# Kernel optimization log

Hardware: AMD Instinct MI355X
Metric: run time of the kernel (lower is better)

The kernel has to match this reference:

```python
import jax, jax.numpy as jnp
import numpy as np

N, C, S, K, H, ES, L = 50000, 128, 2048, 64, 128, 256, 5
E = S * ES


def setup_inputs() -> dict:
    key = jax.random.key(0)
    ks = jax.random.split(key, 16)
    lin = lambda k_, i, o: jax.random.normal(k_, (i, o), jnp.float32) * 0.02
    inp = {}
    inp["x"] = jax.random.normal(ks[0], (N, C), jnp.float32)
    inp["log_probs"] = jax.random.normal(ks[1], (S,), jnp.float32)
    inp["node_proj_w"] = lin(ks[2], C, H); inp["node_proj_b"] = jnp.zeros(H, jnp.float32)
    inp["logp_proj_w"] = lin(ks[3], 1, H); inp["logp_proj_b"] = jnp.zeros(H, jnp.float32)
    inp["root_emb"] = jax.random.normal(ks[4], (2, H), jnp.float32) * 0.02
    inp["init_proj_w"] = lin(ks[5], 3 * H, H); inp["init_proj_b"] = jnp.zeros(H, jnp.float32)
    inp["gin_eps"] = jnp.zeros(L, jnp.float32)
    inp["mlp_w1"] = jax.random.normal(ks[6], (L, H, H), jnp.float32) * 0.02
    inp["mlp_b1"] = jnp.zeros((L, H), jnp.float32)
    inp["mlp_w2"] = jax.random.normal(ks[7], (L, H, H), jnp.float32) * 0.02
    inp["mlp_b2"] = jnp.zeros((L, H), jnp.float32)
    inp["mp2_w"] = jax.random.normal(ks[8], (L, 2 * H, H), jnp.float32) * 0.02
    inp["mp2_b"] = jnp.zeros((L, H), jnp.float32)
    inp["bn_gamma"] = jnp.ones((L, H), jnp.float32)
    inp["bn_beta"] = jnp.zeros((L, H), jnp.float32)
    inp["nodes_t"] = jax.random.randint(ks[9], (S, K), 0, N, jnp.int32)
    inp["root_local"] = jax.random.randint(ks[10], (S,), 0, K, jnp.int32)
    inp["edge_index_t"] = jax.random.randint(ks[11], (2, E), 0, K, jnp.int32)
    inp["edge_ptr"] = jnp.arange(S + 1, dtype=jnp.int32) * ES  # uniform ES edges/subgraph
    return inp


def reference(x, log_probs, node_proj_w, node_proj_b, logp_proj_w, logp_proj_b,
              root_emb, init_proj_w, init_proj_b, gin_eps, mlp_w1, mlp_b1,
              mlp_w2, mlp_b2, mp2_w, mp2_b, bn_gamma, bn_beta,
              nodes_t, root_local, edge_index_t, edge_ptr):
    S_, K_ = nodes_t.shape
    N_total = x.shape[0]
    ids = nodes_t.reshape(-1)                      # [S*k] global IDs, -1 = pad
    valid = ids >= 0
    vf = valid.astype(x.dtype)[:, None]            # [S*k,1]
    idc = jnp.maximum(ids, 0)

    # ---- initial features: node_proj(x_v) || logp_proj(log_p) || root_emb ----
    gx = x[idc] * vf                               # [S*k,C]
    lp = jnp.repeat(log_probs, K_)[:, None]        # [S*k,1]
    root_flat = jnp.arange(S_, dtype=jnp.int32) * K_ + root_local
    root_mask = jnp.zeros(S_ * K_, jnp.int32).at[root_flat].set(1)
    h_node = gx @ node_proj_w + node_proj_b
    h_logp = lp @ logp_proj_w + logp_proj_b
    h_root = root_emb[root_mask]
    h = jnp.concatenate([h_node, h_logp, h_root], axis=-1) @ init_proj_w + init_proj_b

    # ---- intra-subgraph edge index in the flat S*k node space ----
    eidx = jnp.arange(edge_index_t.shape[1], dtype=jnp.int32)
    sub_of_edge = jnp.searchsorted(edge_ptr, eidx, side='right').astype(jnp.int32) - 1
    offs = sub_of_edge * K_
    src = edge_index_t[0] + offs
    dst = edge_index_t[1] + offs

    # valid-node counts per original-graph node (for scatter-mean)
    cnt = jax.ops.segment_sum(vf[:, 0], idc, num_segments=N_total)
    inv_cnt = (1.0 / jnp.maximum(cnt, 1.0))[:, None]

    for l in range(L):
        h_res = h
        # MP-1: GINConv  out = MLP((1+eps)*h + sum_{j->i} h_j)
        agg = jax.ops.segment_sum(h[src], dst, num_segments=S_ * K_)
        z = (1.0 + gin_eps[l]) * h + agg
        z = jax.nn.relu(z @ mlp_w1[l] + mlp_b1[l]) @ mlp_w2[l] + mlp_b2[l]
        # MP-2: cross-subgraph scatter-mean over global node IDs, gather back
        x_agg = jax.ops.segment_sum(z * vf, idc, num_segments=N_total) * inv_cnt
        x_cross = x_agg[idc] * vf
        u = jax.nn.relu(jnp.concatenate([z, x_cross], axis=-1) @ mp2_w[l] + mp2_b[l])
        # BatchNorm (batch statistics, biased var)
        mu = u.mean(axis=0)
        var = u.var(axis=0)
        u = (u - mu) * jax.lax.rsqrt(var + 1e-5) * bn_gamma[l] + bn_beta[l]
        h = u + h_res  # residual; dropout is identity in deterministic reference
    return h
```

## Files before the change

kernel.cpp:

```cpp
#include <hip/hip_runtime.h>
#include <cstdint>

#define NN   50000
#define SS   2048
#define KSUB 64
#define HH   128
#define EE   (SS * 256)
#define SKK  (SS * KSUB)
#define LLAY 5
#define NBLK 196

typedef __attribute__((ext_vector_type(8))) short bhalf8;
typedef __attribute__((ext_vector_type(4))) float f32x4;

__device__ __forceinline__ ushort f2b(float f) {
  uint u = __builtin_bit_cast(uint, f);
  uint r = (u + 0x7FFFu + ((u >> 16) & 1u)) >> 16;
  return (ushort)r;
}
__device__ __forceinline__ float b2f(ushort u) {
  uint v = ((uint)u) << 16;
  return __builtin_bit_cast(float, v);
}
__device__ __forceinline__ void fsplit(float f, ushort& hi, ushort& lo) {
  hi = f2b(f);
  lo = f2b(f - b2f(hi));
}
__device__ __forceinline__ int zoff(int row, int col) {
  return row * 256 + (((col * 2) & 255) ^ ((row & 7) << 4));
}

__global__ void fold_M_k(const float* __restrict__ Wn, const float* __restrict__ Wi,
                         ushort* __restrict__ Mth, ushort* __restrict__ Mtl) {
  int c = blockIdx.x, n = threadIdx.x;
  float s = 0.f;
  for (int k = 0; k < HH; ++k) s = fmaf(Wn[c * HH + k], Wi[k * HH + n], s);
  ushort hi, lo; fsplit(s, hi, lo);
  Mth[n * HH + c] = hi; Mtl[n * HH + c] = lo;
}

__global__ void fold_vec_k(const float* __restrict__ Wi, const float* __restrict__ wl,
                           const float* __restrict__ bnb, const float* __restrict__ blb,
                           const float* __restrict__ bi, const float* __restrict__ remb,
                           float* __restrict__ vl, float* __restrict__ c0,
                           float* __restrict__ rev) {
  int n = threadIdx.x;
  float svl = 0.f, sc0 = bi[n], r0 = 0.f, r1 = 0.f;
  for (int k = 0; k < HH; ++k) {
    svl = fmaf(wl[k], Wi[(HH + k) * HH + n], svl);
    sc0 = fmaf(bnb[k], Wi[k * HH + n], sc0);
    sc0 = fmaf(blb[k], Wi[(HH + k) * HH + n], sc0);
    r0  = fmaf(remb[k],      Wi[(2 * HH + k) * HH + n], r0);
    r1  = fmaf(remb[HH + k], Wi[(2 * HH + k) * HH + n], r1);
  }
  vl[n] = svl; c0[n] = sc0; rev[n] = r0; rev[HH + n] = r1;
}

__global__ void wconv_k(const float* __restrict__ w1, const float* __restrict__ w2,
                        const float* __restrict__ mp2w,
                        ushort* __restrict__ w1th, ushort* __restrict__ w1tl,
                        ushort* __restrict__ w2th, ushort* __restrict__ w2tl,
                        ushort* __restrict__ mp2th, ushort* __restrict__ mp2tl) {
  int b = blockIdx.x, n = threadIdx.x;
  ushort hi, lo;
  if (b < 640) {
    int l = b >> 7, k = b & 127;
    fsplit(w1[((size_t)l * HH + k) * HH + n], hi, lo);
    w1th[((size_t)l * HH + n) * HH + k] = hi;
    w1tl[((size_t)l * HH + n) * HH + k] = lo;
  } else if (b < 1280) {
    int bb = b - 640; int l = bb >> 7, k = bb & 127;
    fsplit(w2[((size_t)l * HH + k) * HH + n], hi, lo);
    w2th[((size_t)l * HH + n) * HH + k] = hi;
    w2tl[((size_t)l * HH + n) * HH + k] = lo;
  } else {
    int bb = b - 1280; int l = bb >> 8, k = bb & 255;
    fsplit(mp2w[((size_t)l * 256 + k) * HH + n], hi, lo);
    mp2th[((size_t)l * HH + n) * 256 + k] = hi;
    mp2tl[((size_t)l * HH + n) * 256 + k] = lo;
  }
}

__global__ void count_k(const int* __restrict__ idc, int* __restrict__ cnt) {
  int i = blockIdx.x * 256 + threadIdx.x;
  if (i < SKK) atomicAdd(&cnt[idc[i]], 1);
}

__global__ void scan1_k(const int* __restrict__ cnt, int* __restrict__ excl,
                        int* __restrict__ bsum) {
  __shared__ int sh[256];
  const int tid = threadIdx.x;
  const int i = blockIdx.x * 256 + tid;
  int v = (i < NN) ? cnt[i] : 0;
  sh[tid] = v;
  __syncthreads();
#pragma unroll
  for (int off = 1; off < 256; off <<= 1) {
    int t = (tid >= off) ? sh[tid - off] : 0;
    __syncthreads();
    sh[tid] += t;
    __syncthreads();
  }
  excl[i] = sh[tid] - v;
  if (tid == 255) bsum[blockIdx.x] = sh[tid];
}

__global__ void scan2_k(int* __restrict__ bsum, int* __restrict__ boff) {
  __shared__ int sh[256];
  const int tid = threadIdx.x;
  int v = (tid < NBLK) ? bsum[tid] : 0;
  sh[tid] = v;
  __syncthreads();
#pragma unroll
  for (int off = 1; off < 256; off <<= 1) {
    int t = (tid >= off) ? sh[tid - off] : 0;
    __syncthreads();
    sh[tid] += t;
    __syncthreads();
  }
  boff[tid] = sh[tid] - v;
}

__global__ void scan3_k(const int* __restrict__ excl, const int* __restrict__ boff,
                        int* __restrict__ node_ptr) {
  int i = blockIdx.x * 256 + threadIdx.x;
  if (i < NN) node_ptr[i] = excl[i] + boff[blockIdx.x];
  if (i == 0) node_ptr[NN] = SKK;
}

__global__ void fill_rows_k(const int* __restrict__ idc, const int* __restrict__ node_ptr,
                            int* __restrict__ cur, int* __restrict__ rowlist) {
  int i = blockIdx.x * 256 + threadIdx.x;
  if (i < SKK) {
    int id = idc[i];
    int pos = atomicAdd(&cur[id], 1);
    rowlist[node_ptr[id] + pos] = i;
  }
}

__launch_bounds__(256)
__global__ void scatter_mean_k(const ushort* __restrict__ zh, const ushort* __restrict__ zl,
                               const int* __restrict__ node_ptr,
                               const int* __restrict__ rowlist,
                               ushort* __restrict__ xah, ushort* __restrict__ xal) {
  const int tid = threadIdx.x;
  const int n = blockIdx.x * 8 + (tid >> 5);
  if (n >= NN) return;
  const int c4 = (tid & 31) * 4;
  const int p0 = node_ptr[n], p1 = node_ptr[n + 1];
  float s0 = 0.f, s1 = 0.f, s2 = 0.f, s3 = 0.f;
  for (int p = p0; p < p1; ++p) {
    const size_t off = (size_t)rowlist[p] * HH + c4;
    uint2 vh = *(const uint2*)(zh + off);
    uint2 vl = *(const uint2*)(zl + off);
    s0 += b2f((ushort)vh.x) + b2f((ushort)vl.x);
    s1 += b2f((ushort)(vh.x >> 16)) + b2f((ushort)(vl.x >> 16));
    s2 += b2f((ushort)vh.y) + b2f((ushort)vl.y);
    s3 += b2f((ushort)(vh.y >> 16)) + b2f((ushort)(vl.y >> 16));
  }
  const float inv = 1.0f / (float)max(p1 - p0, 1);
  ushort h0, l0, h1, l1, h2, l2, h3, l3;
  fsplit(s0 * inv, h0, l0); fsplit(s1 * inv, h1, l1);
  fsplit(s2 * inv, h2, l2); fsplit(s3 * inv, h3, l3);
  uint2 oh, ol;
  oh.x = (uint)h0 | ((uint)h1 << 16); oh.y = (uint)h2 | ((uint)h3 << 16);
  ol.x = (uint)l0 | ((uint)l1 << 16); ol.y = (uint)l2 | ((uint)l3 << 16);
  *(uint2*)(xah + (size_t)n * HH + c4) = oh;
  *(uint2*)(xal + (size_t)n * HH + c4) = ol;
}

__launch_bounds__(256)
__global__ void presort_k(const int* __restrict__ e_src, const int* __restrict__ e_dst,
                          const int* __restrict__ edge_ptr, int* __restrict__ row_ptr,
                          int* __restrict__ ssrc) {
  __shared__ int cnt[KSUB];
  __shared__ int base[KSUB];
  __shared__ int cur[KSUB];
  const int s = blockIdx.x, tid = threadIdx.x;
  const int p0 = edge_ptr[s], p1 = edge_ptr[s + 1];
  if (tid < KSUB) cnt[tid] = 0;
  __syncthreads();
  for (int e = p0 + tid; e < p1; e += 256) atomicAdd(&cnt[e_dst[e]], 1);
  __syncthreads();
  if (tid == 0) {
    int a = 0;
    for (int d = 0; d < KSUB; ++d) { base[d] = a; a += cnt[d]; }
  }
  __syncthreads();
  if (tid < KSUB) { row_ptr[s * KSUB + tid] = p0 + base[tid]; cur[tid] = base[tid]; }
  if (s == 0 && tid == 0) row_ptr[SS * KSUB] = edge_ptr[SS];
  __syncthreads();
  for (int e = p0 + tid; e < p1; e += 256) {
    int d = e_dst[e];
    int pos = atomicAdd(&cur[d], 1);
    ssrc[p0 + pos] = e_src[e];
  }
}

template <bool FIRST>
__launch_bounds__(256, 4)
__global__ void gin_mega_k(float* __restrict__ h, const float* __restrict__ uf,
                           const float* __restrict__ stats,
                           const float* __restrict__ gamma, const float* __restrict__ beta,
                           const int* __restrict__ row_ptr, const int* __restrict__ ssrc,
                           const float* __restrict__ gin_eps, const int layer,
                           const ushort* __restrict__ B1h, const ushort* __restrict__ B1l,
                           const ushort* __restrict__ B2h, const ushort* __restrict__ B2l,
                           const float* __restrict__ bias1, const float* __restrict__ bias2,
                           ushort* __restrict__ zh, ushort* __restrict__ zl) {
  constexpr int LDH = 132;
  __shared__ __align__(16) char smem[KSUB * LDH * 4];
  float*  hl = (float*)smem;
  ushort* Zh = (ushort*)smem;
  ushort* Zl = (ushort*)(smem + KSUB * HH * 2);
  const int s = blockIdx.x, tid = threadIdx.x;
  const size_t base = (size_t)s * KSUB * HH;

  float csc[4], csh[4];
  const int cb = (tid * 4) & 127;
  if constexpr (!FIRST) {
    const float invM = 1.0f / (float)SKK;
#pragma unroll
    for (int e = 0; e < 4; ++e) {
      const float mu = stats[cb + e] * invM;
      const float var = fmaf(-mu, mu, stats[HH + cb + e] * invM);
      const float sc = rsqrtf(var + 1e-5f) * gamma[cb + e];
      csc[e] = sc; csh[e] = fmaf(-mu, sc, beta[cb + e]);
    }
  }
#pragma unroll
  for (int it = 0; it < 8; ++it) {
    const int idx = it * 1024 + tid * 4;
    const int m = idx >> 7, c = idx & 127;
    float4 hv = *(const float4*)&h[base + idx];
    if constexpr (!FIRST) {
      float4 u4 = *(const float4*)&uf[base + idx];
      hv.x += fmaf(u4.x, csc[0], csh[0]);
      hv.y += fmaf(u4.y, csc[1], csh[1]);
      hv.z += fmaf(u4.z, csc[2], csh[2]);
      hv.w += fmaf(u4.w, csc[3], csh[3]);
      *(float4*)&h[base + idx] = hv;
    }
    *(float4*)&hl[m * LDH + c] = hv;
  }
  __syncthreads();

  const float ep1 = 1.0f + gin_eps[layer];
  const int d = tid >> 2, q4 = (tid & 3) * 4;
  const int g = s * KSUB + d;
  const int e0 = row_ptr[g], e1 = row_ptr[g + 1];
  float a[32];
  {
    const float* hp0 = &hl[d * LDH + q4];
#pragma unroll
    for (int j = 0; j < 8; ++j) {
      float4 v = *(const float4*)(hp0 + 16 * j);
      a[4 * j + 0] = ep1 * v.x; a[4 * j + 1] = ep1 * v.y;
      a[4 * j + 2] = ep1 * v.z; a[4 * j + 3] = ep1 * v.w;
    }
    for (int e = e0; e < e1; ++e) {
      const float* hp = &hl[ssrc[e] * LDH + q4];
#pragma unroll
      for (int j = 0; j < 8; ++j) {
        float4 v = *(const float4*)(hp + 16 * j);
        a[4 * j + 0] += v.x; a[4 * j + 1] += v.y;
        a[4 * j + 2] += v.z; a[4 * j + 3] += v.w;
      }
    }
  }
  __syncthreads();

#pragma unroll
  for (int j = 0; j < 8; ++j) {
    ushort th[4], tl[4];
#pragma unroll
    for (int k = 0; k < 4; ++k) fsplit(a[4 * j + k], th[k], tl[k]);
    const int o = zoff(d, q4 + 16 * j);
    *(uint2*)((char*)Zh + o) = *(uint2*)th;
    *(uint2*)((char*)Zl + o) = *(uint2*)tl;
  }
  __syncthreads();

  const int lane = tid & 63, wv = tid >> 6;
  const int fr = lane & 15, quad = lane >> 4;
  const int nj0 = wv * 32 + fr, nj1 = nj0 + 16;

  f32x4 acc[4][2];
#pragma unroll
  for (int i = 0; i < 4; ++i) { acc[i][0] = (f32x4){0,0,0,0}; acc[i][1] = (f32x4){0,0,0,0}; }

#pragma unroll
  for (int ch = 0; ch < 4; ++ch) {
    bhalf8 afh[4], afl[4], bfh[2], bfl[2];
#pragma unroll
    for (int i = 0; i < 4; ++i) {
      const int o = zoff(i * 16 + fr, ch * 32 + quad * 8);
      afh[i] = *(const bhalf8*)((const char*)Zh + o);
      afl[i] = *(const bhalf8*)((const char*)Zl + o);
    }
#pragma unroll
    for (int j = 0; j < 2; ++j) {
      const size_t off = (size_t)(wv * 32 + j * 16 + fr) * HH + ch * 32 + quad * 8;
      bfh[j] = *(const bhalf8*)(B1h + off);
      bfl[j] = *(const bhalf8*)(B1l + off);
    }
#pragma unroll
    for (int i = 0; i < 4; ++i)
#pragma unroll
      for (int j = 0; j < 2; ++j) {
        acc[i][j] = __builtin_amdgcn_mfma_f32_16x16x32_bf16(afh[i], bfh[j], acc[i][j], 0, 0, 0);
        acc[i][j] = __builtin_amdgcn_mfma_f32_16x16x32_bf16(afl[i], bfh[j], acc[i][j], 0, 0, 0);
        acc[i][j] = __builtin_amdgcn_mfma_f32_16x16x32_bf16(afh[i], bfl[j], acc[i][j], 0, 0, 0);
      }
  }
  __syncthreads();

  {
    const float b10 = bias1[nj0], b11 = bias1[nj1];
#pragma unroll
    for (int i = 0; i < 4; ++i)
#pragma unroll
      for (int r = 0; r < 4; ++r) {
        const int row = i * 16 + quad * 4 + r;
        const float o0 = fmaxf(acc[i][0][r] + b10, 0.f);
        const float o1 = fmaxf(acc[i][1][r] + b11, 0.f);
        ushort h0, l0, h1, l1; fsplit(o0, h0, l0); fsplit(o1, h1, l1);
        *(ushort*)((char*)Zh + zoff(row, nj0)) = h0;
        *(ushort*)((char*)Zl + zoff(row, nj0)) = l0;
        *(ushort*)((char*)Zh + zoff(row, nj1)) = h1;
        *(ushort*)((char*)Zl + zoff(row, nj1)) = l1;
      }
  }
  __syncthreads();

#pragma unroll
  for (int i = 0; i < 4; ++i) { acc[i][0] = (f32x4){0,0,0,0}; acc[i][1] = (f32x4){0,0,0,0}; }
#pragma unroll
  for (int ch = 0; ch < 4; ++ch) {
    bhalf8 afh[4], afl[4], bfh[2], bfl[2];
#pragma unroll
    for (int i = 0; i < 4; ++i) {
      const int o = zoff(i * 16 + fr, ch * 32 + quad * 8);
      afh[i] = *(const bhalf8*)((const char*)Zh + o);
      afl[i] = *(const bhalf8*)((const char*)Zl + o);
    }
#pragma unroll
    for (int j = 0; j < 2; ++j) {
      const size_t off = (size_t)(wv * 32 + j * 16 + fr) * HH + ch * 32 + quad * 8;
      bfh[j] = *(const bhalf8*)(B2h + off);
      bfl[j] = *(const bhalf8*)(B2l + off);
    }
#pragma unroll
    for (int i = 0; i < 4; ++i)
#pragma unroll
      for (int j = 0; j < 2; ++j) {
        acc[i][j] = __builtin_amdgcn_mfma_f32_16x16x32_bf16(afh[i], bfh[j], acc[i][j], 0, 0, 0);
        acc[i][j] = __builtin_amdgcn_mfma_f32_16x16x32_bf16(afl[i], bfh[j], acc[i][j], 0, 0, 0);
        acc[i][j] = __builtin_amdgcn_mfma_f32_16x16x32_bf16(afh[i], bfl[j], acc[i][j], 0, 0, 0);
      }
  }
  __syncthreads();

  {
    const float b20 = bias2[nj0], b21 = bias2[nj1];
#pragma unroll
    for (int i = 0; i < 4; ++i)
#pragma unroll
      for (int r = 0; r < 4; ++r) {
        const int row = i * 16 + quad * 4 + r;
        const float o0 = acc[i][0][r] + b20;
        const float o1 = acc[i][1][r] + b21;
        ushort h0, l0, h1, l1; fsplit(o0, h0, l0); fsplit(o1, h1, l1);
        *(ushort*)((char*)Zh + zoff(row, nj0)) = h0;
        *(ushort*)((char*)Zl + zoff(row, nj0)) = l0;
        *(ushort*)((char*)Zh + zoff(row, nj1)) = h1;
        *(ushort*)((char*)Zl + zoff(row, nj1)) = l1;
      }
  }
  __syncthreads();

#pragma unroll
  for (int k = 0; k < 4; ++k) {
    const int gidx = tid * 8 + k * 2048;
    const int row = gidx >> 7;
    const int col = gidx & 127;
    const int o = zoff(row, col);
    *(uint4*)(zh + base + gidx) = *(const uint4*)((const char*)Zh + o);
    *(uint4*)(zl + base + gidx) = *(const uint4*)((const char*)Zl + o);
  }
}

__launch_bounds__(256, 3)
__global__ void mp2_k(const ushort* __restrict__ Ah, const ushort* __restrict__ Al,
                      const ushort* __restrict__ A2h, const ushort* __restrict__ A2l,
                      const ushort* __restrict__ Bh, const ushort* __restrict__ Bl,
                      const float* __restrict__ bias, float* __restrict__ Cf,
                      const int* __restrict__ idc, float* __restrict__ stats) {
  constexpr int LDP = 40;
  __shared__ __align__(16) ushort Ash[128 * LDP];
  __shared__ __align__(16) ushort Asl[128 * LDP];
  __shared__ __align__(16) ushort Bsh[128 * LDP];
  __shared__ __align__(16) ushort Bsl[128 * LDP];
  const int tid = threadIdx.x;
  const int row0 = blockIdx.x * 128;
  const int lane = tid & 63, wv = tid >> 6;
  const int wm = (wv >> 1) * 64, wn = (wv & 1) * 64;
  const int fr = lane & 15, quad = lane >> 4;
  const int sr = tid >> 1;
  const int sc = (tid & 1) * 16;
  const int grow = idc[row0 + sr];

  f32x4 acc[4][4];
#pragma unroll
  for (int i = 0; i < 4; ++i)
#pragma unroll
    for (int j = 0; j < 4; ++j) acc[i][j] = (f32x4){0.f, 0.f, 0.f, 0.f};

  uint4 pa0, pa1, pa2, pa3, pb0, pb1, pb2, pb3;
  auto LA = [&](int ch) {
    const ushort *sh_, *sl_;
    if (ch >= 4) {
      const size_t off = (size_t)grow * HH + (ch - 4) * 32 + sc;
      sh_ = A2h + off; sl_ = A2l + off;
    } else {
      const size_t off = (size_t)(row0 + sr) * HH + ch * 32 + sc;
      sh_ = Ah + off; sl_ = Al + off;
    }
    pa0 = *(const uint4*)(sh_);     pa1 = *(const uint4*)(sh_ + 8);
    pa2 = *(const uint4*)(sl_);     pa3 = *(const uint4*)(sl_ + 8);
  };
  auto LB = [&](int ch) {
    const size_t off = (size_t)sr * 256 + ch * 32 + sc;
    pb0 = *(const uint4*)(Bh + off); pb1 = *(const uint4*)(Bh + off + 8);
    pb2 = *(const uint4*)(Bl + off); pb3 = *(const uint4*)(Bl + off + 8);
  };

  LA(0); LB(0);
#pragma unroll
  for (int ch = 0; ch < 8; ++ch) {
    *(uint4*)&Ash[sr * LDP + sc]     = pa0;
    *(uint4*)&Ash[sr * LDP + sc + 8] = pa1;
    *(uint4*)&Asl[sr * LDP + sc]     = pa2;
    *(uint4*)&Asl[sr * LDP + sc + 8] = pa3;
    *(uint4*)&Bsh[sr * LDP + sc]     = pb0;
    *(uint4*)&Bsh[sr * LDP + sc + 8] = pb1;
    *(uint4*)&Bsl[sr * LDP + sc]     = pb2;
    *(uint4*)&Bsl[sr * LDP + sc + 8] = pb3;
    __syncthreads();
    if (ch < 7) { LA(ch + 1); LB(ch + 1); }
    bhalf8 afh[4], afl[4], bfh[4], bfl[4];
#pragma unroll
    for (int i = 0; i < 4; ++i) {
      const int r = (wm + i * 16 + fr) * LDP + quad * 8;
      afh[i] = *(const bhalf8*)&Ash[r];
      afl[i] = *(const bhalf8*)&Asl[r];
    }
#pragma unroll
    for (int j = 0; j < 4; ++j) {
      const int r = (wn + j * 16 + fr) * LDP + quad * 8;
      bfh[j] = *(const bhalf8*)&Bsh[r];
      bfl[j] = *(const bhalf8*)&Bsl[r];
    }
#pragma unroll
    for (int i = 0; i < 4; ++i)
#pragma unroll
      for (int j = 0; j < 4; ++j) {
        acc[i][j] = __builtin_amdgcn_mfma_f32_16x16x32_bf16(afh[i], bfh[j], acc[i][j], 0, 0, 0);
        acc[i][j] = __builtin_amdgcn_mfma_f32_16x16x32_bf16(afl[i], bfh[j], acc[i][j], 0, 0, 0);
        acc[i][j] = __builtin_amdgcn_mfma_f32_16x16x32_bf16(afh[i], bfl[j], acc[i][j], 0, 0, 0);
      }
    __syncthreads();
  }

  const int nj[4] = {wn + fr, wn + 16 + fr, wn + 32 + fr, wn + 48 + fr};
  float bb[4];
#pragma unroll
  for (int j = 0; j < 4; ++j) bb[j] = bias[nj[j]];
  float psum[4] = {0.f, 0.f, 0.f, 0.f}, psq[4] = {0.f, 0.f, 0.f, 0.f};
#pragma unroll
  for (int i = 0; i < 4; ++i)
#pragma unroll
    for (int r = 0; r < 4; ++r) {
      const int m = row0 + wm + i * 16 + quad * 4 + r;
      const size_t base = (size_t)m * HH;
#pragma unroll
      for (int j = 0; j < 4; ++j) {
        float o = fmaxf(acc[i][j][r] + bb[j], 0.f);
        Cf[base + nj[j]] = o;
        psum[j] += o; psq[j] += o * o;
      }
    }
  float* ssum = (float*)Ash;
  float* ssq = ssum + HH;
  if (tid < HH) { ssum[tid] = 0.f; ssq[tid] = 0.f; }
  __syncthreads();
#pragma unroll
  for (int j = 0; j < 4; ++j) {
    atomicAdd(&ssum[nj[j]], psum[j]);
    atomicAdd(&ssq[nj[j]], psq[j]);
  }
  __syncthreads();
  if (tid < HH) {
    unsafeAtomicAdd(&stats[tid], ssum[tid]);
    unsafeAtomicAdd(&stats[HH + tid], ssq[tid]);
  }
}

__launch_bounds__(256, 2)
__global__ void mgemm0_k(const float* __restrict__ Afp,
                         const ushort* __restrict__ Bh, const ushort* __restrict__ Bl,
                         float* __restrict__ Cf,
                         const int* __restrict__ idc, const float* __restrict__ log_probs,
                         const int* __restrict__ root_local, const float* __restrict__ vl,
                         const float* __restrict__ c0v, const float* __restrict__ rev) {
  constexpr int LDP = 40;
  __shared__ __align__(16) ushort Ash[128 * LDP];
  __shared__ __align__(16) ushort Asl[128 * LDP];
  __shared__ __align__(16) ushort Bsh[128 * LDP];
  __shared__ __align__(16) ushort Bsl[128 * LDP];
  const int tid = threadIdx.x;
  const int row0 = blockIdx.x * 128;
  const int lane = tid & 63, wv = tid >> 6;
  const int wm = (wv >> 1) * 64, wn = (wv & 1) * 64;
  const int fr = lane & 15, quad = lane >> 4;
  const int sr = tid >> 1;
  const int sc = (tid & 1) * 16;

  f32x4 acc[4][4];
#pragma unroll
  for (int i = 0; i < 4; ++i)
#pragma unroll
    for (int j = 0; j < 4; ++j) acc[i][j] = (f32x4){0.f, 0.f, 0.f, 0.f};

  for (int ch = 0; ch < 4; ++ch) {
    {
      const float* src = Afp + (size_t)idc[row0 + sr] * HH + ch * 32 + sc;
      float fv[16];
      *(float4*)&fv[0]  = *(const float4*)(src);
      *(float4*)&fv[4]  = *(const float4*)(src + 4);
      *(float4*)&fv[8]  = *(const float4*)(src + 8);
      *(float4*)&fv[12] = *(const float4*)(src + 12);
      ushort hi[16], lo[16];
#pragma unroll
      for (int e = 0; e < 16; ++e) fsplit(fv[e], hi[e], lo[e]);
      *(uint4*)&Ash[sr * LDP + sc]     = *(uint4*)&hi[0];
      *(uint4*)&Ash[sr * LDP + sc + 8] = *(uint4*)&hi[8];
      *(uint4*)&Asl[sr * LDP + sc]     = *(uint4*)&lo[0];
      *(uint4*)&Asl[sr * LDP + sc + 8] = *(uint4*)&lo[8];
    }
    {
      const size_t off = (size_t)sr * HH + ch * 32 + sc;
      *(uint4*)&Bsh[sr * LDP + sc]     = *(const uint4*)(Bh + off);
      *(uint4*)&Bsh[sr * LDP + sc + 8] = *(const uint4*)(Bh + off + 8);
      *(uint4*)&Bsl[sr * LDP + sc]     = *(const uint4*)(Bl + off);
      *(uint4*)&Bsl[sr * LDP + sc + 8] = *(const uint4*)(Bl + off + 8);
    }
    __syncthreads();
    bhalf8 afh[4], afl[4], bfh[4], bfl[4];
#pragma unroll
    for (int i = 0; i < 4; ++i) {
      const int r = (wm + i * 16 + fr) * LDP + quad * 8;
      afh[i] = *(const bhalf8*)&Ash[r];
      afl[i] = *(const bhalf8*)&Asl[r];
    }
#pragma unroll
    for (int j = 0; j < 4; ++j) {
      const int r = (wn + j * 16 + fr) * LDP + quad * 8;
      bfh[j] = *(const bhalf8*)&Bsh[r];
      bfl[j] = *(const bhalf8*)&Bsl[r];
    }
#pragma unroll
    for (int i = 0; i < 4; ++i)
#pragma unroll
      for (int j = 0; j < 4; ++j) {
        acc[i][j] = __builtin_amdgcn_mfma_f32_16x16x32_bf16(afh[i], bfh[j], acc[i][j], 0, 0, 0);
        acc[i][j] = __builtin_amdgcn_mfma_f32_16x16x32_bf16(afl[i], bfh[j], acc[i][j], 0, 0, 0);
        acc[i][j] = __builtin_amdgcn_mfma_f32_16x16x32_bf16(afh[i], bfl[j], acc[i][j], 0, 0, 0);
      }
    __syncthreads();
  }

  const int nj[4] = {wn + fr, wn + 16 + fr, wn + 32 + fr, wn + 48 + fr};
  float c0a[4], vla[4], re0[4], re1[4];
#pragma unroll
  for (int j = 0; j < 4; ++j) {
    c0a[j] = c0v[nj[j]]; vla[j] = vl[nj[j]];
    re0[j] = rev[nj[j]]; re1[j] = rev[HH + nj[j]];
  }
#pragma unroll
  for (int i = 0; i < 4; ++i)
#pragma unroll
    for (int r = 0; r < 4; ++r) {
      const int m = row0 + wm + i * 16 + quad * 4 + r;
      const int s = m >> 6;
      const float lp = log_probs[s];
      const bool isr = (m & 63) == root_local[s];
      const size_t base = (size_t)m * HH;
#pragma unroll
      for (int j = 0; j < 4; ++j)
        Cf[base + nj[j]] = acc[i][j][r] + c0a[j] + lp * vla[j] + (isr ? re1[j] : re0[j]);
    }
}

__launch_bounds__(256)
__global__ void bn_apply_k(const float* __restrict__ u, float* __restrict__ h,
                           const float* __restrict__ stats,
                           const float* __restrict__ gamma, const float* __restrict__ beta) {
  size_t i4 = (size_t)(blockIdx.x * 256 + threadIdx.x) * 4;
  int c = (int)(i4 & 127);
  const float invM = 1.0f / (float)SKK;
  float sc[4], sh[4];
#pragma unroll
  for (int e = 0; e < 4; ++e) {
    const float mu = stats[c + e] * invM;
    const float var = fmaf(-mu, mu, stats[HH + c + e] * invM);
    const float s = rsqrtf(var + 1e-5f) * gamma[c + e];
    sc[e] = s; sh[e] = fmaf(-mu, s, beta[c + e]);
  }
  float4 uv = *(const float4*)(u + i4);
  float4 hv = *(const float4*)(h + i4);
  float4 o;
  o.x = fmaf(uv.x, sc[0], sh[0]) + hv.x;
  o.y = fmaf(uv.y, sc[1], sh[1]) + hv.y;
  o.z = fmaf(uv.z, sc[2], sh[2]) + hv.z;
  o.w = fmaf(uv.w, sc[3], sh[3]) + hv.w;
  *(float4*)(h + i4) = o;
}

extern "C" void kernel_launch(void* const* d_in, const int* in_sizes, int n_in,
                              void* d_out, int out_size, void* d_ws, size_t ws_size,
                              hipStream_t stream) {
  const float* x          = (const float*)d_in[0];
  const float* log_probs  = (const float*)d_in[1];
  const float* node_w     = (const float*)d_in[2];
  const float* node_b     = (const float*)d_in[3];
  const float* logp_w     = (const float*)d_in[4];
  const float* logp_b     = (const float*)d_in[5];
  const float* root_emb   = (const float*)d_in[6];
  const float* init_w     = (const float*)d_in[7];
  const float* init_b     = (const float*)d_in[8];
  const float* gin_eps    = (const float*)d_in[9];
  const float* w1         = (const float*)d_in[10];
  const float* b1         = (const float*)d_in[11];
  const float* w2         = (const float*)d_in[12];
  const float* b2         = (const float*)d_in[13];
  const float* mp2w       = (const float*)d_in[14];
  const float* mp2b       = (const float*)d_in[15];
  const float* gamma      = (const float*)d_in[16];
  const float* beta       = (const float*)d_in[17];
  const int*   nodes      = (const int*)d_in[18];
  const int*   root_local = (const int*)d_in[19];
  const int*   edge_idx   = (const int*)d_in[20];
  const int*   edge_ptr   = (const int*)d_in[21];
  float* h = (float*)d_out;

  char* wp = (char*)d_ws;
  auto take = [&](size_t bytes) { char* p = wp; wp += (bytes + 255) & ~(size_t)255; return p; };
  ushort* zh    = (ushort*)take((size_t)SKK * HH * 2);
  ushort* zl    = (ushort*)take((size_t)SKK * HH * 2);
  float*  uf    = (float*)take((size_t)SKK * HH * 4);
  ushort* xah   = (ushort*)take((size_t)NN * HH * 2);
  ushort* xal   = (ushort*)take((size_t)NN * HH * 2);
  ushort* Mth   = (ushort*)take((size_t)HH * HH * 2);
  ushort* Mtl   = (ushort*)take((size_t)HH * HH * 2);
  ushort* w1th  = (ushort*)take((size_t)LLAY * HH * HH * 2);
  ushort* w1tl  = (ushort*)take((size_t)LLAY * HH * HH * 2);
  ushort* w2th  = (ushort*)take((size_t)LLAY * HH * HH * 2);
  ushort* w2tl  = (ushort*)take((size_t)LLAY * HH * HH * 2);
  ushort* mp2th = (ushort*)take((size_t)LLAY * HH * 256 * 2);
  ushort* mp2tl = (ushort*)take((size_t)LLAY * HH * 256 * 2);
  float* vl       = (float*)take(HH * 4);
  float* c0v      = (float*)take(HH * 4);
  float* rev      = (float*)take(2 * HH * 4);
  float* bn_stats = (float*)take(LLAY * 2 * HH * 4);
  int*   cnti     = (int*)take((size_t)NN * 4);
  int*   excl     = (int*)take((size_t)NBLK * 256 * 4);
  int*   bsum     = (int*)take(256 * 4);
  int*   boff     = (int*)take(256 * 4);
  int*   node_ptr = (int*)take((size_t)(NN + 1) * 4);
  int*   cur      = (int*)take((size_t)NN * 4);
  int*   rowlist  = (int*)take((size_t)SKK * 4);
  int*   row_ptr  = (int*)take((size_t)(SKK + 1) * 4);
  int*   ssrc     = (int*)take((size_t)EE * 4);

  hipMemsetAsync(cnti, 0, (size_t)NN * 4, stream);
  hipMemsetAsync(cur, 0, (size_t)NN * 4, stream);
  hipMemsetAsync(bn_stats, 0, LLAY * 2 * HH * 4, stream);
  fold_M_k<<<HH, HH, 0, stream>>>(node_w, init_w, Mth, Mtl);
  fold_vec_k<<<1, HH, 0, stream>>>(init_w, logp_w, node_b, logp_b, init_b, root_emb,
                                   vl, c0v, rev);
  wconv_k<<<2560, HH, 0, stream>>>(w1, w2, mp2w, w1th, w1tl, w2th, w2tl, mp2th, mp2tl);
  count_k<<<SKK / 256, 256, 0, stream>>>(nodes, cnti);
  scan1_k<<<NBLK, 256, 0, stream>>>(cnti, excl, bsum);
  scan2_k<<<1, 256, 0, stream>>>(bsum, boff);
  scan3_k<<<NBLK, 256, 0, stream>>>(excl, boff, node_ptr);
  fill_rows_k<<<SKK / 256, 256, 0, stream>>>(nodes, node_ptr, cur, rowlist);
  presort_k<<<SS, 256, 0, stream>>>(edge_idx, edge_idx + EE, edge_ptr, row_ptr, ssrc);

  mgemm0_k<<<SKK / 128, 256, 0, stream>>>(x, Mth, Mtl, h,
                                          nodes, log_probs, root_local, vl, c0v, rev);

  for (int l = 0; l < LLAY; ++l) {
    if (l == 0) {
      gin_mega_k<true><<<SS, 256, 0, stream>>>(h, nullptr, nullptr, nullptr, nullptr,
                                               row_ptr, ssrc, gin_eps, l,
                                               w1th + (size_t)l * HH * HH,
                                               w1tl + (size_t)l * HH * HH,
                                               w2th + (size_t)l * HH * HH,
                                               w2tl + (size_t)l * HH * HH,
                                               b1 + l * HH, b2 + l * HH, zh, zl);
    } else {
      gin_mega_k<false><<<SS, 256, 0, stream>>>(h, uf, bn_stats + (l - 1) * 2 * HH,
                                                gamma + (l - 1) * HH, beta + (l - 1) * HH,
                                                row_ptr, ssrc, gin_eps, l,
                                                w1th + (size_t)l * HH * HH,
                                                w1tl + (size_t)l * HH * HH,
                                                w2th + (size_t)l * HH * HH,
                                                w2tl + (size_t)l * HH * HH,
                                                b1 + l * HH, b2 + l * HH, zh, zl);
    }
    scatter_mean_k<<<(NN + 7) / 8, 256, 0, stream>>>(zh, zl, node_ptr, rowlist, xah, xal);
    mp2_k<<<SKK / 128, 256, 0, stream>>>(zh, zl, xah, xal,
                                         mp2th + (size_t)l * HH * 256,
                                         mp2tl + (size_t)l * HH * 256,
                                         mp2b + l * HH, uf, nodes,
                                         bn_stats + l * 2 * HH);
  }
  bn_apply_k<<<(SKK * HH / 4) / 256, 256, 0, stream>>>(uf, h, bn_stats + 4 * 2 * HH,
                                                       gamma + 4 * HH, beta + 4 * HH);
}
```

Before: 992.3 us.

## Stage subgraph edge sources in LDS and prefetch next chunk in mgemm0

The GIN aggregation kernel now copies each subgraph's sorted source indices into shared memory once, so the per-edge inner loop reads them from LDS instead of global memory. The first-layer gather GEMM hoists the row index load and register-prefetches the next K-chunk of A and B while MFMAs run on the current chunk, overlapping global latency with compute. Its launch bounds are raised to three blocks per SM, which limits registers per thread and may cause spills given the added prefetch registers. The LDS index buffer assumes at most 256 edges per subgraph.

```diff
diff --git a/kernel.cpp b/kernel.cpp
--- a/kernel.cpp
+++ b/kernel.cpp
@@ -210,11 +210,19 @@
                            ushort* __restrict__ zh, ushort* __restrict__ zl) {
   constexpr int LDH = 132;
   __shared__ __align__(16) char smem[KSUB * LDH * 4];
+  __shared__ int ssrc_lds[256];
   float*  hl = (float*)smem;
   ushort* Zh = (ushort*)smem;
   ushort* Zl = (ushort*)(smem + KSUB * HH * 2);
   const int s = blockIdx.x, tid = threadIdx.x;
   const size_t base = (size_t)s * KSUB * HH;
+
+  const int e_start = row_ptr[s * KSUB];
+  {
+    const int e_end = row_ptr[s * KSUB + KSUB];
+    for (int e = e_start + tid; e < e_end; e += 256)
+      ssrc_lds[e - e_start] = ssrc[e];
+  }
 
   float csc[4], csh[4];
   const int cb = (tid * 4) & 127;
@@ -259,7 +267,7 @@
       a[4 * j + 2] = ep1 * v.z; a[4 * j + 3] = ep1 * v.w;
     }
     for (int e = e0; e < e1; ++e) {
-      const float* hp = &hl[ssrc[e] * LDH + q4];
+      const float* hp = &hl[ssrc_lds[e - e_start] * LDH + q4];
 #pragma unroll
       for (int j = 0; j < 8; ++j) {
         float4 v = *(const float4*)(hp + 16 * j);
@@ -506,7 +514,7 @@
   }
 }
 
-__launch_bounds__(256, 2)
+__launch_bounds__(256, 3)
 __global__ void mgemm0_k(const float* __restrict__ Afp,
                          const ushort* __restrict__ Bh, const ushort* __restrict__ Bl,
                          float* __restrict__ Cf,
@@ -525,6 +533,7 @@
   const int fr = lane & 15, quad = lane >> 4;
   const int sr = tid >> 1;
   const int sc = (tid & 1) * 16;
+  const int arow = idc[row0 + sr];
 
   f32x4 acc[4][4];
 #pragma unroll
@@ -532,14 +541,26 @@
 #pragma unroll
     for (int j = 0; j < 4; ++j) acc[i][j] = (f32x4){0.f, 0.f, 0.f, 0.f};
 
+  float4 pf0, pf1, pf2, pf3;
+  uint4  pb0, pb1, pb2, pb3;
+  auto LA = [&](int ch) {
+    const float* src = Afp + (size_t)arow * HH + ch * 32 + sc;
+    pf0 = *(const float4*)(src);     pf1 = *(const float4*)(src + 4);
+    pf2 = *(const float4*)(src + 8); pf3 = *(const float4*)(src + 12);
+  };
+  auto LB = [&](int ch) {
+    const size_t off = (size_t)sr * HH + ch * 32 + sc;
+    pb0 = *(const uint4*)(Bh + off); pb1 = *(const uint4*)(Bh + off + 8);
+    pb2 = *(const uint4*)(Bl + off); pb3 = *(const uint4*)(Bl + off + 8);
+  };
+
+  LA(0); LB(0);
+#pragma unroll
   for (int ch = 0; ch < 4; ++ch) {
     {
-      const float* src = Afp + (size_t)idc[row0 + sr] * HH + ch * 32 + sc;
       float fv[16];
-      *(float4*)&fv[0]  = *(const float4*)(src);
-      *(float4*)&fv[4]  = *(const float4*)(src + 4);
-      *(float4*)&fv[8]  = *(const float4*)(src + 8);
-      *(float4*)&fv[12] = *(const float4*)(src + 12);
+      *(float4*)&fv[0]  = pf0; *(float4*)&fv[4]  = pf1;
+      *(float4*)&fv[8]  = pf2; *(float4*)&fv[12] = pf3;
       ushort hi[16], lo[16];
 #pragma unroll
       for (int e = 0; e < 16; ++e) fsplit(fv[e], hi[e], lo[e]);
@@ -548,14 +569,12 @@
       *(uint4*)&Asl[sr * LDP + sc]     = *(uint4*)&lo[0];
       *(uint4*)&Asl[sr * LDP + sc + 8] = *(uint4*)&lo[8];
     }
-    {
-      const size_t off = (size_t)sr * HH + ch * 32 + sc;
-      *(uint4*)&Bsh[sr * LDP + sc]     = *(const uint4*)(Bh + off);
-      *(uint4*)&Bsh[sr * LDP + sc + 8] = *(const uint4*)(Bh + off + 8);
-      *(uint4*)&Bsl[sr * LDP + sc]     = *(const uint4*)(Bl + off);
-      *(uint4*)&Bsl[sr * LDP + sc + 8] = *(const uint4*)(Bl + off + 8);
-    }
+    *(uint4*)&Bsh[sr * LDP + sc]     = pb0;
+    *(uint4*)&Bsh[sr * LDP + sc + 8] = pb1;
+    *(uint4*)&Bsl[sr * LDP + sc]     = pb2;
+    *(uint4*)&Bsl[sr * LDP + sc + 8] = pb3;
     __syncthreads();
+    if (ch < 3) { LA(ch + 1); LB(ch + 1); }
     bhalf8 afh[4], afl[4], bfh[4], bfl[4];
 #pragma unroll
     for (int i = 0; i < 4; ++i) {
```

New measurement: 990.1 us. About the same (-0.2%).
